# Performance work log

Measured on AMD Instinct MI355X. Metric: run time of the kernel, lower is better.

## Reference

```python
import jax, jax.numpy as jnp
import numpy as np

EMBED_DIM = 512
NUM_HEADS = 8
HEAD_DIM = EMBED_DIM // NUM_HEADS  # 64


def setup_inputs() -> dict:
    key = jax.random.key(0)
    ks = jax.random.split(key, 9)
    B, N, E, H, D = 4, 1024, EMBED_DIM, NUM_HEADS, HEAD_DIM
    s = 1.0 / np.sqrt(E)  # ~ nn.Linear init scale
    x = jax.random.normal(ks[0], (B, N, E), dtype=jnp.float32)
    # weights stored as (in, out): y = x @ W + b (same math as torch x @ W.T)
    Wq = jax.random.uniform(ks[1], (E, E), jnp.float32, -s, s)
    bq = jax.random.uniform(ks[2], (E,), jnp.float32, -s, s)
    Wk = jax.random.uniform(ks[3], (E, E), jnp.float32, -s, s)
    bk = jax.random.uniform(ks[4], (E,), jnp.float32, -s, s)
    Wv = jax.random.uniform(ks[5], (E, E), jnp.float32, -s, s)
    bv = jax.random.uniform(ks[6], (E,), jnp.float32, -s, s)
    Wg = jax.random.uniform(ks[7], (E, H * D * D), jnp.float32, -s, s)
    bg = jax.random.uniform(ks[8], (H * D * D,), jnp.float32, -s, s)
    return {"x": x, "Wq": Wq, "bq": bq, "Wk": Wk, "bk": bk,
            "Wv": Wv, "bv": bv, "Wg": Wg, "bg": bg}


def reference(x, Wq, bq, Wk, bk, Wv, bv, Wg, bg):
    B, N, E = x.shape
    H, D = NUM_HEADS, HEAD_DIM
    # per-token generated transform g: [B, N, H, D, D] (act = exact GELU)
    g = jax.nn.gelu(x @ Wg + bg, approximate=False).reshape(B, N, H, D, D)
    q = (x @ Wq + bq).reshape(B, N, H, D)
    k = (x @ Wk + bk).reshape(B, N, H, D)
    v = (x @ Wv + bv).reshape(B, N, H, D)
    # q' = q @ g  (per-token, per-head 1xD @ DxD)
    qg = jnp.einsum("bnhd,bnhde->bnhe", q, g)
    # attention scores (note: no 1/sqrt(d) scaling in the original)
    att = jnp.einsum("bnhe,bmhe->bhnm", qg, k)
    att = jax.nn.softmax(att, axis=-1)
    out = jnp.einsum("bhnm,bmhd->bnhd", att, v)
    return out.reshape(B, N, E)
```

## Files before the change

kernel.cpp:

```cpp
#include <hip/hip_runtime.h>
#include <math.h>

#define TOK   4096
#define EDIM  512
#define HEADS 8
#define DHEAD 64
#define GCOLS 32768

typedef unsigned short u16;
typedef _Float16 f16;
typedef __attribute__((ext_vector_type(8))) f16 f16x8;
typedef __attribute__((ext_vector_type(4))) f16 f16x4;
typedef __attribute__((ext_vector_type(4))) float f32x4;
typedef __attribute__((ext_vector_type(4))) unsigned short u16x4;

typedef const __attribute__((address_space(1))) void* gas_ptr;
typedef __attribute__((address_space(3))) void* las_ptr;

__device__ __forceinline__ void gll16(const void* g, void* lds) {
  __builtin_amdgcn_global_load_lds((gas_ptr)g, (las_ptr)lds, 16, 0, 0);
}

__device__ __forceinline__ u16 f2h_bits(float f) {
  union { f16 h; u16 u; } v; v.h = (f16)f;
  return v.u;
}

__device__ __forceinline__ float fast_gelu(float x) {
  float s = x * 0.7071067811865475f;
  float ax = fabsf(s);
  float t = 1.0f / (1.0f + 0.3275911f * ax);
  float poly = t * (0.254829592f + t * (-0.284496736f + t * (1.421413741f +
               t * (-1.453152027f + t * 1.061405429f))));
  float e = __expf(-ax * ax);
  float r = 1.0f - poly * e;
  float erfv = copysignf(r, s);
  return 0.5f * x * (1.0f + erfv);
}

__global__ void cast_f16_k(const float* __restrict__ in, u16* __restrict__ out, int n) {
  int i = (blockIdx.x * blockDim.x + threadIdx.x) * 4;
  if (i + 3 < n) {
    float4 f = *(const float4*)(in + i);
    u16x4 h;
    h.x = f2h_bits(f.x); h.y = f2h_bits(f.y);
    h.z = f2h_bits(f.z); h.w = f2h_bits(f.w);
    *(u16x4*)(out + i) = h;
  }
}

__global__ void transpose_f16_k(const float* __restrict__ in, u16* __restrict__ out,
                                int K, int N) {
  __shared__ float tile[32][33];
  int n0 = blockIdx.x * 32, k0 = blockIdx.y * 32;
  int tx = threadIdx.x, ty = threadIdx.y;
  #pragma unroll
  for (int i = 0; i < 4; i++)
    tile[ty + i * 8][tx] = in[(size_t)(k0 + ty + i * 8) * N + n0 + tx];
  __syncthreads();
  #pragma unroll
  for (int i = 0; i < 4; i++)
    out[(size_t)(n0 + ty + i * 8) * K + k0 + tx] = f2h_bits(tile[tx][ty + i * 8]);
}

__global__ __launch_bounds__(256, 2) void qkv_gemm_k(
    const u16* __restrict__ xf, const u16* __restrict__ Wqt,
    const u16* __restrict__ Wkt, const u16* __restrict__ Wvt,
    const float* __restrict__ bq, const float* __restrict__ bk, const float* __restrict__ bv,
    u16* __restrict__ qho, u16* __restrict__ ko, u16* __restrict__ vTo) {
  __shared__ __align__(16) u16 As[16 * 512];
  __shared__ __align__(16) u16 Bs[16 * 512];
  const int which = blockIdx.z;
  const u16* Wt = which == 0 ? Wqt : (which == 1 ? Wkt : Wvt);
  const float* bias = which == 0 ? bq : (which == 1 ? bk : bv);
  const int m0 = blockIdx.x * 128;
  const int n0 = blockIdx.y * 128;
  const int tid = threadIdx.x;
  const int w = tid >> 6, lane = tid & 63, l15 = lane & 15, quad = lane >> 4;
  const int mhalf = w >> 1, nhalf = w & 1;

  f32x4 acc[4][4];
  #pragma unroll
  for (int i = 0; i < 4; i++)
    #pragma unroll
    for (int j = 0; j < 4; j++) acc[i][j] = f32x4{0.f, 0.f, 0.f, 0.f};

  for (int kk = 0; kk < 512; kk += 64) {
    #pragma unroll
    for (int i = 0; i < 8; i++) {
      int cb = w * 8 + i;
      if (cb < 16) {
        int ks = cb >> 3, mt = cb & 7;
        gll16(xf + (size_t)(m0 + mt * 16 + l15) * 512 + kk + ks * 32 + quad * 8,
              As + cb * 512);
      } else {
        int bi = cb - 16, ks = bi >> 3, nt = bi & 7;
        gll16(Wt + (size_t)(n0 + nt * 16 + l15) * 512 + kk + ks * 32 + quad * 8,
              Bs + bi * 512);
      }
    }
    __syncthreads();
    #pragma unroll
    for (int ks = 0; ks < 2; ks++) {
      f16x8 a[4], b[4];
      #pragma unroll
      for (int mt = 0; mt < 4; mt++)
        a[mt] = *(const f16x8*)(As + (ks * 8 + mhalf * 4 + mt) * 512 + lane * 8);
      #pragma unroll
      for (int nt = 0; nt < 4; nt++)
        b[nt] = *(const f16x8*)(Bs + (ks * 8 + nhalf * 4 + nt) * 512 + lane * 8);
      #pragma unroll
      for (int mt = 0; mt < 4; mt++)
        #pragma unroll
        for (int nt = 0; nt < 4; nt++)
          acc[mt][nt] = __builtin_amdgcn_mfma_f32_16x16x32_f16(a[mt], b[nt], acc[mt][nt], 0, 0, 0);
    }
    __syncthreads();
  }
  #pragma unroll
  for (int nt = 0; nt < 4; nt++) {
    int col = n0 + (nhalf * 4 + nt) * 16 + l15;
    float bia = bias[col];
    int h = col >> 6, d = col & 63;
    #pragma unroll
    for (int mt = 0; mt < 4; mt++) {
      #pragma unroll
      for (int r = 0; r < 4; r++) {
        int t = m0 + (mhalf * 4 + mt) * 16 + quad * 4 + r;
        int b_ = t >> 10, n = t & 1023;
        float val = acc[mt][nt][r] + bia;
        size_t idx = (((size_t)(b_ * 8 + h) * 1024) + n) * 64 + d;
        if (which == 0)      qho[idx] = f2h_bits(val);
        else if (which == 1) ko[idx] = f2h_bits(val);
        else                 vTo[(((size_t)(b_ * 8 + h) * 64) + d) * 1024 + n] = f2h_bits(val);
      }
    }
  }
}

__global__ __launch_bounds__(512, 4) void qg_fused_k(
    const u16* __restrict__ xf, const u16* __restrict__ Wgt,
    const float* __restrict__ bg, const u16* __restrict__ qh,
    float* __restrict__ qgp) {
  __shared__ __align__(16) u16 As[16 * 512];
  __shared__ __align__(16) u16 Bs[32 * 512];
  __shared__ __align__(16) u16 Qs[128 * 64];
  const int head = blockIdx.x & 7;
  const int jh = (blockIdx.x >> 3) & 1;
  const int t0 = (blockIdx.x >> 4) * 128;
  const int tid = threadIdx.x;
  const int w = tid >> 6, lane = tid & 63, l15 = lane & 15, quad = lane >> 4;
  const int mhalf = w >> 2;
  const int ntA = w & 3;
  const int b_ = t0 >> 10, nseq0 = t0 & 1023;
  const u16* qbase = qh + (((size_t)(b_ * 8 + head) * 1024) + nseq0) * 64;

  #pragma unroll
  for (int i = 0; i < 2; i++) {
    int cb = w * 2 + i;
    gll16(qbase + (size_t)cb * 512 + (size_t)lane * 8, Qs + (size_t)cb * 512);
  }
  f32x4 qg[4];
  #pragma unroll
  for (int i = 0; i < 4; i++) qg[i] = f32x4{0.f, 0.f, 0.f, 0.f};
  __syncthreads();

  for (int jp = 0; jp < 8; jp++) {
    const int j0 = jh * 16 + jp * 2;
    const int c0 = head * 4096 + j0 * 128;
    f32x4 zacc[4][4];
    #pragma unroll
    for (int i = 0; i < 4; i++)
      #pragma unroll
      for (int z = 0; z < 4; z++) zacc[i][z] = f32x4{0.f, 0.f, 0.f, 0.f};

    for (int kk = 0; kk < 512; kk += 64) {
      #pragma unroll
      for (int i = 0; i < 6; i++) {
        int cb = w * 6 + i;
        if (cb < 16) {
          int ks = cb >> 3, mt = cb & 7;
          gll16(xf + (size_t)(t0 + mt * 16 + l15) * 512 + kk + ks * 32 + quad * 8,
                As + cb * 512);
        } else {
          int bi = cb - 16, ks = bi >> 4, nt = bi & 15;
          gll16(Wgt + (size_t)(c0 + nt * 16 + l15) * 512 + kk + ks * 32 + quad * 8,
                Bs + bi * 512);
        }
      }
      __syncthreads();
      #pragma unroll
      for (int ks = 0; ks < 2; ks++) {
        f16x8 a[4];
        #pragma unroll
        for (int mt = 0; mt < 4; mt++)
          a[mt] = *(const f16x8*)(As + (ks * 8 + mhalf * 4 + mt) * 512 + lane * 8);
        #pragma unroll
        for (int z = 0; z < 4; z++) {
          int nt = (z >> 1) * 8 + (z & 1) * 4 + ntA;
          f16x8 b = *(const f16x8*)(Bs + (ks * 16 + nt) * 512 + lane * 8);
          #pragma unroll
          for (int mt = 0; mt < 4; mt++)
            zacc[mt][z] = __builtin_amdgcn_mfma_f32_16x16x32_f16(a[mt], b, zacc[mt][z], 0, 0, 0);
        }
      }
      __syncthreads();
    }
    float bgv[4];
    #pragma unroll
    for (int z = 0; z < 4; z++) {
      int nt = (z >> 1) * 8 + (z & 1) * 4 + ntA;
      bgv[z] = bg[c0 + nt * 16 + l15];
    }
    const int d0 = 2 * j0;
    #pragma unroll
    for (int mt = 0; mt < 4; mt++) {
      #pragma unroll
      for (int r = 0; r < 4; r++) {
        int row = mhalf * 64 + mt * 16 + quad * 4 + r;
        f16x4 qp = *(const f16x4*)(Qs + row * 64 + d0);
        float g0 = fast_gelu(zacc[mt][0][r] + bgv[0]);
        float g1 = fast_gelu(zacc[mt][1][r] + bgv[1]);
        float g2 = fast_gelu(zacc[mt][2][r] + bgv[2]);
        float g3 = fast_gelu(zacc[mt][3][r] + bgv[3]);
        qg[mt][r] += (float)qp.x * g0 + (float)qp.y * g1 +
                     (float)qp.z * g2 + (float)qp.w * g3;
      }
    }
  }
  float* qout = qgp + (size_t)jh * TOK * EDIM;
  const int eb = ntA * 16;
  #pragma unroll
  for (int mt = 0; mt < 4; mt++) {
    #pragma unroll
    for (int r = 0; r < 4; r++) {
      int t = t0 + mhalf * 64 + mt * 16 + quad * 4 + r;
      int bb = t >> 10, n = t & 1023;
      qout[(((size_t)(bb * 8 + head) * 1024) + n) * 64 + eb + l15] = qg[mt][r];
    }
  }
}

__global__ __launch_bounds__(256, 2) void attn_k(
    const float* __restrict__ qgp, const u16* __restrict__ kb,
    const u16* __restrict__ vTb, float* __restrict__ out) {
  __shared__ __align__(16) u16 Ks[8 * 512];
  __shared__ __align__(16) u16 Vs[8 * 512];
  __shared__ __align__(16) f16 Ps[4][16 * 72];
  const int idx = blockIdx.x;
  const int bh = idx & 31;
  const int qt = idx >> 5;
  const int b_ = bh >> 3, h = bh & 7;
  const int tid = threadIdx.x;
  const int w = tid >> 6, lane = tid & 63, l15 = lane & 15, quad = lane >> 4;

  const float* qg0 = qgp + (size_t)bh * 1024 * 64;
  const float* qg1 = qg0 + (size_t)TOK * EDIM;
  const u16* kB  = kb  + (size_t)bh * 1024 * 64;
  const u16* vB  = vTb + (size_t)bh * 64 * 1024;

  f16x8 aq[2];
  #pragma unroll
  for (int ks = 0; ks < 2; ks++) {
    size_t off = (size_t)(qt * 64 + w * 16 + l15) * 64 + ks * 32 + quad * 8;
    f16x8 v;
    #pragma unroll
    for (int e = 0; e < 8; e++)
      v[e] = (f16)(qg0[off + e] + qg1[off + e]);
    aq[ks] = v;
  }

  f32x4 o[4];
  #pragma unroll
  for (int i = 0; i < 4; i++) o[i] = f32x4{0.f, 0.f, 0.f, 0.f};
  float m_old[4], l_old[4];
  #pragma unroll
  for (int r = 0; r < 4; r++) { m_old[r] = -1e30f; l_old[r] = 0.f; }

  for (int kt = 0; kt < 16; kt++) {
    #pragma unroll
    for (int i = 0; i < 2; i++) {
      int cb = w * 2 + i;
      int ks = cb >> 2, nt = cb & 3;
      gll16(kB + (size_t)(kt * 64 + nt * 16 + l15) * 64 + ks * 32 + quad * 8, Ks + cb * 512);
      gll16(vB + (size_t)(nt * 16 + l15) * 1024 + kt * 64 + ks * 32 + quad * 8, Vs + cb * 512);
    }
    __syncthreads();
    f32x4 s[4];
    #pragma unroll
    for (int nt = 0; nt < 4; nt++) s[nt] = f32x4{0.f, 0.f, 0.f, 0.f};
    #pragma unroll
    for (int ks = 0; ks < 2; ks++)
      #pragma unroll
      for (int nt = 0; nt < 4; nt++) {
        f16x8 kf = *(const f16x8*)(Ks + (ks * 4 + nt) * 512 + lane * 8);
        s[nt] = __builtin_amdgcn_mfma_f32_16x16x32_f16(aq[ks], kf, s[nt], 0, 0, 0);
      }
    float rmax[4];
    #pragma unroll
    for (int r = 0; r < 4; r++)
      rmax[r] = fmaxf(fmaxf(s[0][r], s[1][r]), fmaxf(s[2][r], s[3][r]));
    #pragma unroll
    for (int off = 1; off < 16; off <<= 1)
      #pragma unroll
      for (int r = 0; r < 4; r++)
        rmax[r] = fmaxf(rmax[r], __shfl_xor(rmax[r], off));
    float alpha[4], rsum[4];
    #pragma unroll
    for (int r = 0; r < 4; r++) {
      float mn = fmaxf(m_old[r], rmax[r]);
      alpha[r] = __expf(m_old[r] - mn);
      m_old[r] = mn;
      rsum[r] = 0.f;
    }
    #pragma unroll
    for (int nt = 0; nt < 4; nt++)
      #pragma unroll
      for (int r = 0; r < 4; r++) {
        float p = __expf(s[nt][r] - m_old[r]);
        rsum[r] += p;
        Ps[w][(quad * 4 + r) * 72 + nt * 16 + l15] = (f16)p;
      }
    #pragma unroll
    for (int off = 1; off < 16; off <<= 1)
      #pragma unroll
      for (int r = 0; r < 4; r++)
        rsum[r] += __shfl_xor(rsum[r], off);
    #pragma unroll
    for (int r = 0; r < 4; r++) l_old[r] = l_old[r] * alpha[r] + rsum[r];
    #pragma unroll
    for (int nt = 0; nt < 4; nt++)
      #pragma unroll
      for (int r = 0; r < 4; r++) o[nt][r] *= alpha[r];
    #pragma unroll
    for (int ks = 0; ks < 2; ks++) {
      f16x8 pa = *(const f16x8*)(&Ps[w][l15 * 72 + ks * 32 + quad * 8]);
      #pragma unroll
      for (int nt = 0; nt < 4; nt++) {
        f16x8 vf = *(const f16x8*)(Vs + (ks * 4 + nt) * 512 + lane * 8);
        o[nt] = __builtin_amdgcn_mfma_f32_16x16x32_f16(pa, vf, o[nt], 0, 0, 0);
      }
    }
    __syncthreads();
  }
  #pragma unroll
  for (int r = 0; r < 4; r++) {
    float inv = 1.f / l_old[r];
    int n = qt * 64 + w * 16 + quad * 4 + r;
    #pragma unroll
    for (int nt = 0; nt < 4; nt++)
      out[((size_t)(b_ * 1024 + n)) * 512 + h * 64 + nt * 16 + l15] = o[nt][r] * inv;
  }
}

extern "C" void kernel_launch(void* const* d_in, const int* in_sizes, int n_in,
                              void* d_out, int out_size, void* d_ws, size_t ws_size,
                              hipStream_t stream) {
  const float* x  = (const float*)d_in[0];
  const float* Wq = (const float*)d_in[1];
  const float* bq = (const float*)d_in[2];
  const float* Wk = (const float*)d_in[3];
  const float* bk = (const float*)d_in[4];
  const float* Wv = (const float*)d_in[5];
  const float* bv = (const float*)d_in[6];
  const float* Wg = (const float*)d_in[7];
  const float* bg = (const float*)d_in[8];
  float* out = (float*)d_out;

  const size_t NX = (size_t)TOK * EDIM;
  const size_t NWG = (size_t)GCOLS * EDIM;
  const size_t NW = (size_t)EDIM * EDIM;

  char* p = (char*)d_ws;
  u16* xf  = (u16*)p; p += NX * 2;
  u16* Wgt = (u16*)p; p += NWG * 2;
  u16* Wqt = (u16*)p; p += NW * 2;
  u16* Wkt = (u16*)p; p += NW * 2;
  u16* Wvt = (u16*)p; p += NW * 2;
  u16* qh  = (u16*)p; p += NX * 2;
  u16* kf  = (u16*)p; p += NX * 2;
  u16* vT  = (u16*)p; p += NX * 2;
  float* qgp = (float*)p; p += NX * 4 * 2;

  hipLaunchKernelGGL(cast_f16_k, dim3(NX / 1024), dim3(256), 0, stream,
                     x, xf, (int)NX);
  hipLaunchKernelGGL(transpose_f16_k, dim3(EDIM / 32, EDIM / 32), dim3(32, 8), 0, stream,
                     Wq, Wqt, EDIM, EDIM);
  hipLaunchKernelGGL(transpose_f16_k, dim3(EDIM / 32, EDIM / 32), dim3(32, 8), 0, stream,
                     Wk, Wkt, EDIM, EDIM);
  hipLaunchKernelGGL(transpose_f16_k, dim3(EDIM / 32, EDIM / 32), dim3(32, 8), 0, stream,
                     Wv, Wvt, EDIM, EDIM);
  hipLaunchKernelGGL(transpose_f16_k, dim3(GCOLS / 32, EDIM / 32), dim3(32, 8), 0, stream,
                     Wg, Wgt, EDIM, GCOLS);
  hipLaunchKernelGGL(qkv_gemm_k, dim3(TOK / 128, EDIM / 128, 3), dim3(256), 0, stream,
                     xf, Wqt, Wkt, Wvt, bq, bk, bv, qh, kf, vT);
  hipLaunchKernelGGL(qg_fused_k, dim3(512), dim3(512), 0, stream,
                     xf, Wgt, bg, qh, qgp);
  hipLaunchKernelGGL(attn_k, dim3(512), dim3(256), 0, stream,
                     qgp, kf, vT, out);
}
```

Measured before the change: 482.7 us.

## Double-buffer LDS tiles in all GEMMs and drop split-j partial qg outputs

Adds double-buffered LDS staging to the QKV GEMM, the fused Wg GEMM+GELU+qg kernel and the attention kernel, so the next tile's global-to-LDS load is issued before the current tile's MFMAs. The qg kernel no longer splits the j range across two blocks. Each block covers all 32 column groups for its head in one flattened 128-step loop and writes qg directly as fp16, so attention no longer reads and sums two fp32 partials. GELU uses a hardware reciprocal. The grid for the dominant kernel halves to 256 blocks and LDS per block roughly doubles, which lowers parallelism and occupancy on a chip with many CUs.

```diff
diff --git a/kernel.cpp b/kernel.cpp
--- a/kernel.cpp
+++ b/kernel.cpp
@@ -29,7 +29,7 @@
 __device__ __forceinline__ float fast_gelu(float x) {
   float s = x * 0.7071067811865475f;
   float ax = fabsf(s);
-  float t = 1.0f / (1.0f + 0.3275911f * ax);
+  float t = __builtin_amdgcn_rcpf(1.0f + 0.3275911f * ax);
   float poly = t * (0.254829592f + t * (-0.284496736f + t * (1.421413741f +
                t * (-1.453152027f + t * 1.061405429f))));
   float e = __expf(-ax * ax);
@@ -68,8 +68,8 @@
     const u16* __restrict__ Wkt, const u16* __restrict__ Wvt,
     const float* __restrict__ bq, const float* __restrict__ bk, const float* __restrict__ bv,
     u16* __restrict__ qho, u16* __restrict__ ko, u16* __restrict__ vTo) {
-  __shared__ __align__(16) u16 As[16 * 512];
-  __shared__ __align__(16) u16 Bs[16 * 512];
+  __shared__ __align__(16) u16 As[2][16 * 512];
+  __shared__ __align__(16) u16 Bs[2][16 * 512];
   const int which = blockIdx.z;
   const u16* Wt = which == 0 ? Wqt : (which == 1 ? Wkt : Wvt);
   const float* bias = which == 0 ? bq : (which == 1 ? bk : bv);
@@ -85,30 +85,38 @@
     #pragma unroll
     for (int j = 0; j < 4; j++) acc[i][j] = f32x4{0.f, 0.f, 0.f, 0.f};
 
-  for (int kk = 0; kk < 512; kk += 64) {
+  auto stage = [&](int d, int kk) {
     #pragma unroll
     for (int i = 0; i < 8; i++) {
       int cb = w * 8 + i;
       if (cb < 16) {
         int ks = cb >> 3, mt = cb & 7;
         gll16(xf + (size_t)(m0 + mt * 16 + l15) * 512 + kk + ks * 32 + quad * 8,
-              As + cb * 512);
+              As[d] + cb * 512);
       } else {
         int bi = cb - 16, ks = bi >> 3, nt = bi & 7;
         gll16(Wt + (size_t)(n0 + nt * 16 + l15) * 512 + kk + ks * 32 + quad * 8,
-              Bs + bi * 512);
-      }
-    }
-    __syncthreads();
+              Bs[d] + bi * 512);
+      }
+    }
+  };
+
+  stage(0, 0);
+  __syncthreads();
+  int cur = 0;
+  for (int kt = 0; kt < 8; kt++) {
+    if (kt < 7) stage(cur ^ 1, (kt + 1) * 64);
+    const u16* Asb = As[cur];
+    const u16* Bsb = Bs[cur];
     #pragma unroll
     for (int ks = 0; ks < 2; ks++) {
       f16x8 a[4], b[4];
       #pragma unroll
       for (int mt = 0; mt < 4; mt++)
-        a[mt] = *(const f16x8*)(As + (ks * 8 + mhalf * 4 + mt) * 512 + lane * 8);
+        a[mt] = *(const f16x8*)(Asb + (ks * 8 + mhalf * 4 + mt) * 512 + lane * 8);
       #pragma unroll
       for (int nt = 0; nt < 4; nt++)
-        b[nt] = *(const f16x8*)(Bs + (ks * 8 + nhalf * 4 + nt) * 512 + lane * 8);
+        b[nt] = *(const f16x8*)(Bsb + (ks * 8 + nhalf * 4 + nt) * 512 + lane * 8);
       #pragma unroll
       for (int mt = 0; mt < 4; mt++)
         #pragma unroll
@@ -116,6 +124,7 @@
           acc[mt][nt] = __builtin_amdgcn_mfma_f32_16x16x32_f16(a[mt], b[nt], acc[mt][nt], 0, 0, 0);
     }
     __syncthreads();
+    cur ^= 1;
   }
   #pragma unroll
   for (int nt = 0; nt < 4; nt++) {
@@ -138,16 +147,15 @@
   }
 }
 
-__global__ __launch_bounds__(512, 4) void qg_fused_k(
+__global__ __launch_bounds__(512, 2) void qg_fused_k(
     const u16* __restrict__ xf, const u16* __restrict__ Wgt,
     const float* __restrict__ bg, const u16* __restrict__ qh,
-    float* __restrict__ qgp) {
-  __shared__ __align__(16) u16 As[16 * 512];
-  __shared__ __align__(16) u16 Bs[32 * 512];
+    u16* __restrict__ qg16) {
+  __shared__ __align__(16) u16 As[2][16 * 512];
+  __shared__ __align__(16) u16 Bs[2][32 * 512];
   __shared__ __align__(16) u16 Qs[128 * 64];
   const int head = blockIdx.x & 7;
-  const int jh = (blockIdx.x >> 3) & 1;
-  const int t0 = (blockIdx.x >> 4) * 128;
+  const int t0 = (blockIdx.x >> 3) * 128;
   const int tid = threadIdx.x;
   const int w = tid >> 6, lane = tid & 63, l15 = lane & 15, quad = lane >> 4;
   const int mhalf = w >> 2;
@@ -160,75 +168,88 @@
     int cb = w * 2 + i;
     gll16(qbase + (size_t)cb * 512 + (size_t)lane * 8, Qs + (size_t)cb * 512);
   }
+
+  auto stage = [&](int d, int s) {
+    int jp = s >> 3, kk = (s & 7) << 6;
+    int c0 = head * 4096 + jp * 256;
+    #pragma unroll
+    for (int i = 0; i < 6; i++) {
+      int cb = w * 6 + i;
+      if (cb < 16) {
+        int ks = cb >> 3, mt = cb & 7;
+        gll16(xf + (size_t)(t0 + mt * 16 + l15) * 512 + kk + ks * 32 + quad * 8,
+              As[d] + cb * 512);
+      } else {
+        int bi = cb - 16, ks = bi >> 4, nt = bi & 15;
+        gll16(Wgt + (size_t)(c0 + nt * 16 + l15) * 512 + kk + ks * 32 + quad * 8,
+              Bs[d] + bi * 512);
+      }
+    }
+  };
+
   f32x4 qg[4];
   #pragma unroll
   for (int i = 0; i < 4; i++) qg[i] = f32x4{0.f, 0.f, 0.f, 0.f};
+  f32x4 zacc[4][4];
+  #pragma unroll
+  for (int i = 0; i < 4; i++)
+    #pragma unroll
+    for (int z = 0; z < 4; z++) zacc[i][z] = f32x4{0.f, 0.f, 0.f, 0.f};
+
+  stage(0, 0);
   __syncthreads();
-
-  for (int jp = 0; jp < 8; jp++) {
-    const int j0 = jh * 16 + jp * 2;
-    const int c0 = head * 4096 + j0 * 128;
-    f32x4 zacc[4][4];
-    #pragma unroll
-    for (int i = 0; i < 4; i++)
-      #pragma unroll
-      for (int z = 0; z < 4; z++) zacc[i][z] = f32x4{0.f, 0.f, 0.f, 0.f};
-
-    for (int kk = 0; kk < 512; kk += 64) {
-      #pragma unroll
-      for (int i = 0; i < 6; i++) {
-        int cb = w * 6 + i;
-        if (cb < 16) {
-          int ks = cb >> 3, mt = cb & 7;
-          gll16(xf + (size_t)(t0 + mt * 16 + l15) * 512 + kk + ks * 32 + quad * 8,
-                As + cb * 512);
-        } else {
-          int bi = cb - 16, ks = bi >> 4, nt = bi & 15;
-          gll16(Wgt + (size_t)(c0 + nt * 16 + l15) * 512 + kk + ks * 32 + quad * 8,
-                Bs + bi * 512);
-        }
-      }
-      __syncthreads();
-      #pragma unroll
-      for (int ks = 0; ks < 2; ks++) {
-        f16x8 a[4];
+  int cur = 0;
+  for (int s = 0; s < 128; s++) {
+    if (s < 127) stage(cur ^ 1, s + 1);
+    const u16* Asb = As[cur];
+    const u16* Bsb = Bs[cur];
+    #pragma unroll
+    for (int ks = 0; ks < 2; ks++) {
+      f16x8 a[4];
+      #pragma unroll
+      for (int mt = 0; mt < 4; mt++)
+        a[mt] = *(const f16x8*)(Asb + (ks * 8 + mhalf * 4 + mt) * 512 + lane * 8);
+      #pragma unroll
+      for (int z = 0; z < 4; z++) {
+        int nt = (z >> 1) * 8 + (z & 1) * 4 + ntA;
+        f16x8 b = *(const f16x8*)(Bsb + (ks * 16 + nt) * 512 + lane * 8);
         #pragma unroll
         for (int mt = 0; mt < 4; mt++)
-          a[mt] = *(const f16x8*)(As + (ks * 8 + mhalf * 4 + mt) * 512 + lane * 8);
+          zacc[mt][z] = __builtin_amdgcn_mfma_f32_16x16x32_f16(a[mt], b, zacc[mt][z], 0, 0, 0);
+      }
+    }
+    if ((s & 7) == 7) {
+      int jp = s >> 3;
+      int c0 = head * 4096 + jp * 256;
+      float bgv[4];
+      #pragma unroll
+      for (int z = 0; z < 4; z++) {
+        int nt = (z >> 1) * 8 + (z & 1) * 4 + ntA;
+        bgv[z] = bg[c0 + nt * 16 + l15];
+      }
+      const int d0 = 4 * jp;
+      #pragma unroll
+      for (int mt = 0; mt < 4; mt++) {
         #pragma unroll
-        for (int z = 0; z < 4; z++) {
-          int nt = (z >> 1) * 8 + (z & 1) * 4 + ntA;
-          f16x8 b = *(const f16x8*)(Bs + (ks * 16 + nt) * 512 + lane * 8);
-          #pragma unroll
-          for (int mt = 0; mt < 4; mt++)
-            zacc[mt][z] = __builtin_amdgcn_mfma_f32_16x16x32_f16(a[mt], b, zacc[mt][z], 0, 0, 0);
+        for (int r = 0; r < 4; r++) {
+          int row = mhalf * 64 + mt * 16 + quad * 4 + r;
+          f16x4 qp = *(const f16x4*)(Qs + row * 64 + d0);
+          float g0 = fast_gelu(zacc[mt][0][r] + bgv[0]);
+          float g1 = fast_gelu(zacc[mt][1][r] + bgv[1]);
+          float g2 = fast_gelu(zacc[mt][2][r] + bgv[2]);
+          float g3 = fast_gelu(zacc[mt][3][r] + bgv[3]);
+          qg[mt][r] += (float)qp.x * g0 + (float)qp.y * g1 +
+                       (float)qp.z * g2 + (float)qp.w * g3;
         }
       }
-      __syncthreads();
-    }
-    float bgv[4];
-    #pragma unroll
-    for (int z = 0; z < 4; z++) {
-      int nt = (z >> 1) * 8 + (z & 1) * 4 + ntA;
-      bgv[z] = bg[c0 + nt * 16 + l15];
-    }
-    const int d0 = 2 * j0;
-    #pragma unroll
-    for (int mt = 0; mt < 4; mt++) {
-      #pragma unroll
-      for (int r = 0; r < 4; r++) {
-        int row = mhalf * 64 + mt * 16 + quad * 4 + r;
-        f16x4 qp = *(const f16x4*)(Qs + row * 64 + d0);
-        float g0 = fast_gelu(zacc[mt][0][r] + bgv[0]);
-        float g1 = fast_gelu(zacc[mt][1][r] + bgv[1]);
-        float g2 = fast_gelu(zacc[mt][2][r] + bgv[2]);
-        float g3 = fast_gelu(zacc[mt][3][r] + bgv[3]);
-        qg[mt][r] += (float)qp.x * g0 + (float)qp.y * g1 +
-                     (float)qp.z * g2 + (float)qp.w * g3;
-      }
-    }
-  }
-  float* qout = qgp + (size_t)jh * TOK * EDIM;
+      #pragma unroll
+      for (int i = 0; i < 4; i++)
+        #pragma unroll
+        for (int z = 0; z < 4; z++) zacc[i][z] = f32x4{0.f, 0.f, 0.f, 0.f};
+    }
+    __syncthreads();
+    cur ^= 1;
+  }
   const int eb = ntA * 16;
   #pragma unroll
   for (int mt = 0; mt < 4; mt++) {
@@ -236,16 +257,16 @@
     for (int r = 0; r < 4; r++) {
       int t = t0 + mhalf * 64 + mt * 16 + quad * 4 + r;
       int bb = t >> 10, n = t & 1023;
-      qout[(((size_t)(bb * 8 + head) * 1024) + n) * 64 + eb + l15] = qg[mt][r];
+      qg16[(((size_t)(bb * 8 + head) * 1024) + n) * 64 + eb + l15] = f2h_bits(qg[mt][r]);
     }
   }
 }
 
 __global__ __launch_bounds__(256, 2) void attn_k(
-    const float* __restrict__ qgp, const u16* __restrict__ kb,
+    const u16* __restrict__ qg16, const u16* __restrict__ kb,
     const u16* __restrict__ vTb, float* __restrict__ out) {
-  __shared__ __align__(16) u16 Ks[8 * 512];
-  __shared__ __align__(16) u16 Vs[8 * 512];
+  __shared__ __align__(16) u16 Ks[2][8 * 512];
+  __shared__ __align__(16) u16 Vs[2][8 * 512];
   __shared__ __align__(16) f16 Ps[4][16 * 72];
   const int idx = blockIdx.x;
   const int bh = idx & 31;
@@ -254,21 +275,14 @@
   const int tid = threadIdx.x;
   const int w = tid >> 6, lane = tid & 63, l15 = lane & 15, quad = lane >> 4;
 
-  const float* qg0 = qgp + (size_t)bh * 1024 * 64;
-  const float* qg1 = qg0 + (size_t)TOK * EDIM;
+  const u16* qgB = qg16 + (size_t)bh * 1024 * 64;
   const u16* kB  = kb  + (size_t)bh * 1024 * 64;
   const u16* vB  = vTb + (size_t)bh * 64 * 1024;
 
   f16x8 aq[2];
   #pragma unroll
-  for (int ks = 0; ks < 2; ks++) {
-    size_t off = (size_t)(qt * 64 + w * 16 + l15) * 64 + ks * 32 + quad * 8;
-    f16x8 v;
-    #pragma unroll
-    for (int e = 0; e < 8; e++)
-      v[e] = (f16)(qg0[off + e] + qg1[off + e]);
-    aq[ks] = v;
-  }
+  for (int ks = 0; ks < 2; ks++)
+    aq[ks] = *(const f16x8*)(qgB + (size_t)(qt * 64 + w * 16 + l15) * 64 + ks * 32 + quad * 8);
 
   f32x4 o[4];
   #pragma unroll
@@ -277,15 +291,21 @@
   #pragma unroll
   for (int r = 0; r < 4; r++) { m_old[r] = -1e30f; l_old[r] = 0.f; }
 
-  for (int kt = 0; kt < 16; kt++) {
+  auto stageKV = [&](int d, int kt) {
     #pragma unroll
     for (int i = 0; i < 2; i++) {
       int cb = w * 2 + i;
       int ks = cb >> 2, nt = cb & 3;
-      gll16(kB + (size_t)(kt * 64 + nt * 16 + l15) * 64 + ks * 32 + quad * 8, Ks + cb * 512);
-      gll16(vB + (size_t)(nt * 16 + l15) * 1024 + kt * 64 + ks * 32 + quad * 8, Vs + cb * 512);
-    }
-    __syncthreads();
+      gll16(kB + (size_t)(kt * 64 + nt * 16 + l15) * 64 + ks * 32 + quad * 8, Ks[d] + cb * 512);
+      gll16(vB + (size_t)(nt * 16 + l15) * 1024 + kt * 64 + ks * 32 + quad * 8, Vs[d] + cb * 512);
+    }
+  };
+
+  stageKV(0, 0);
+  __syncthreads();
+  int cur = 0;
+  for (int kt = 0; kt < 16; kt++) {
+    if (kt < 15) stageKV(cur ^ 1, kt + 1);
     f32x4 s[4];
     #pragma unroll
     for (int nt = 0; nt < 4; nt++) s[nt] = f32x4{0.f, 0.f, 0.f, 0.f};
@@ -293,7 +313,7 @@
     for (int ks = 0; ks < 2; ks++)
       #pragma unroll
       for (int nt = 0; nt < 4; nt++) {
-        f16x8 kf = *(const f16x8*)(Ks + (ks * 4 + nt) * 512 + lane * 8);
+        f16x8 kf = *(const f16x8*)(Ks[cur] + (ks * 4 + nt) * 512 + lane * 8);
         s[nt] = __builtin_amdgcn_mfma_f32_16x16x32_f16(aq[ks], kf, s[nt], 0, 0, 0);
       }
     float rmax[4];
@@ -337,11 +357,12 @@
       f16x8 pa = *(const f16x8*)(&Ps[w][l15 * 72 + ks * 32 + quad * 8]);
       #pragma unroll
       for (int nt = 0; nt < 4; nt++) {
-        f16x8 vf = *(const f16x8*)(Vs + (ks * 4 + nt) * 512 + lane * 8);
+        f16x8 vf = *(const f16x8*)(Vs[cur] + (ks * 4 + nt) * 512 + lane * 8);
         o[nt] = __builtin_amdgcn_mfma_f32_16x16x32_f16(pa, vf, o[nt], 0, 0, 0);
       }
     }
     __syncthreads();
+    cur ^= 1;
   }
   #pragma unroll
   for (int r = 0; r < 4; r++) {
@@ -380,7 +401,7 @@
   u16* qh  = (u16*)p; p += NX * 2;
   u16* kf  = (u16*)p; p += NX * 2;
   u16* vT  = (u16*)p; p += NX * 2;
-  float* qgp = (float*)p; p += NX * 4 * 2;
+  u16* qg16 = (u16*)p; p += NX * 2;
 
   hipLaunchKernelGGL(cast_f16_k, dim3(NX / 1024), dim3(256), 0, stream,
                      x, xf, (int)NX);
@@ -394,8 +415,8 @@
                      Wg, Wgt, EDIM, GCOLS);
   hipLaunchKernelGGL(qkv_gemm_k, dim3(TOK / 128, EDIM / 128, 3), dim3(256), 0, stream,
                      xf, Wqt, Wkt, Wvt, bq, bk, bv, qh, kf, vT);
-  hipLaunchKernelGGL(qg_fused_k, dim3(512), dim3(512), 0, stream,
-                     xf, Wgt, bg, qh, qgp);
+  hipLaunchKernelGGL(qg_fused_k, dim3(256), dim3(512), 0, stream,
+                     xf, Wgt, bg, qh, qg16);
   hipLaunchKernelGGL(attn_k, dim3(512), dim3(256), 0, stream,
-                     qgp, kf, vT, out);
-}
+                     qg16, kf, vT, out);
+}
```

New measurement: 472.5 us. 1.02x faster.
